# Kernel optimization log

Measured on AMD Instinct MI355X. Metric: run time of the kernel, lower is better.

Reference implementation:

```python
import jax, jax.numpy as jnp
import numpy as np

B, T, C, H = 2, 2048, 1024, 16
D = C // H  # head dim 64

def setup_inputs() -> dict:
    key = jax.random.key(0)
    k1, k2, k3 = jax.random.split(key, 3)
    x = jax.random.normal(k1, (B, T, C), dtype=jnp.float32)
    W_attn = jax.random.normal(k2, (C, 3 * C), dtype=jnp.float32) * (1.0 / np.sqrt(C))
    b_attn = jnp.zeros((3 * C,), dtype=jnp.float32)
    W_proj = jax.random.normal(k3, (C, C), dtype=jnp.float32) * (1.0 / np.sqrt(C))
    b_proj = jnp.zeros((C,), dtype=jnp.float32)
    return {"x": x, "W_attn": W_attn, "b_attn": b_attn, "W_proj": W_proj, "b_proj": b_proj}

def reference(x, W_attn, b_attn, W_proj, b_proj):
    Bsz, Tlen, Cdim = x.shape
    qkv = x @ W_attn + b_attn  # [B,T,3C]
    q, k, v = jnp.split(qkv, 3, axis=2)
    # [B,T,C] -> [B,H,T,D]
    q = q.reshape(Bsz, Tlen, H, D).transpose(0, 2, 1, 3)
    k = k.reshape(Bsz, Tlen, H, D).transpose(0, 2, 1, 3)
    v = v.reshape(Bsz, Tlen, H, D).transpose(0, 2, 1, 3)
    att = jnp.einsum('bhqd,bhkd->bhqk', q, k) * (1.0 / np.sqrt(D))
    causal = jnp.tril(jnp.ones((Tlen, Tlen), dtype=bool))
    att = jnp.where(causal[None, None, :, :], att, jnp.float32(-jnp.inf))
    att = jax.nn.softmax(att, axis=-1)
    y = jnp.einsum('bhqk,bhkd->bhqd', att, v)  # [B,H,T,D]
    y = y.transpose(0, 2, 1, 3).reshape(Bsz, Tlen, Cdim)
    return y @ W_proj + b_proj
```

## Files before the change

kernel.cpp:

```cpp
#include <hip/hip_runtime.h>
#include <math.h>

#define BSZ 2
#define TSEQ 2048
#define CDIM 1024
#define HNUM 16

typedef __attribute__((ext_vector_type(8))) short bhalf8;
typedef __attribute__((ext_vector_type(4))) short bhalf4;
typedef __attribute__((ext_vector_type(4))) float floatx4;

__device__ __forceinline__ unsigned short f2bf(float f) {
    union { float f; unsigned u; } v;
    v.f = f;
    unsigned r = v.u + 0x7FFFu + ((v.u >> 16) & 1u);
    return (unsigned short)(r >> 16);
}

__device__ __forceinline__ floatx4 fx4_zero() { floatx4 z = {0.f,0.f,0.f,0.f}; return z; }

typedef __attribute__((address_space(3))) unsigned int lds_u32;
typedef const __attribute__((address_space(1))) unsigned int g_u32;
__device__ __forceinline__ void async_copy16(const void* g, void* l) {
    __builtin_amdgcn_global_load_lds((g_u32*)g, (lds_u32*)l, 16, 0, 0);
}

__device__ __forceinline__ void trans_tile(
    const float* __restrict__ W, unsigned short* __restrict__ Wt,
    int K, int N, int n0, int k0, int tid, float (*t)[33])
{
    const int tx = tid & 31, ty = tid >> 5;
#pragma unroll
    for (int i = 0; i < 4; ++i)
        t[ty + i * 8][tx] = W[(size_t)(k0 + ty + i * 8) * N + n0 + tx];
    __syncthreads();
#pragma unroll
    for (int i = 0; i < 4; ++i)
        Wt[(size_t)(n0 + ty + i * 8) * K + k0 + tx] = f2bf(t[tx][ty + i * 8]);
}

__global__ __launch_bounds__(256) void prepass(
    const float* __restrict__ x, unsigned short* __restrict__ xb,
    const float* __restrict__ Wa, unsigned short* __restrict__ WtA,
    const float* __restrict__ Wp, unsigned short* __restrict__ WtP)
{
    __shared__ float t[32][33];
    const int bid = blockIdx.x;
    const int tid = threadIdx.x;
    if (bid < 2048) {
        size_t i = ((size_t)bid * 256 + tid) * 8;
        float4 a = *(const float4*)(x + i);
        float4 b = *(const float4*)(x + i + 4);
        uint4 o;
        o.x = (unsigned)f2bf(a.x) | ((unsigned)f2bf(a.y) << 16);
        o.y = (unsigned)f2bf(a.z) | ((unsigned)f2bf(a.w) << 16);
        o.z = (unsigned)f2bf(b.x) | ((unsigned)f2bf(b.y) << 16);
        o.w = (unsigned)f2bf(b.z) | ((unsigned)f2bf(b.w) << 16);
        *(uint4*)(xb + i) = o;
    } else if (bid < 5120) {
        int tl = bid - 2048;
        trans_tile(Wa, WtA, 1024, 3072, (tl % 96) * 32, (tl / 96) * 32, tid, t);
    } else {
        int tl = bid - 5120;
        trans_tile(Wp, WtP, 1024, 1024, (tl % 32) * 32, (tl / 32) * 32, tid, t);
    }
}

template<int BM, bool OUT_BF16>
__global__ __launch_bounds__(256) void gemm_bt(
    const unsigned short* __restrict__ A, const unsigned short* __restrict__ Bt,
    const float* __restrict__ bias, void* __restrict__ Cp,
    int M, int N, int K, int v_start, unsigned short* __restrict__ vt)
{
    constexpr int ALINES = BM / 64;
    constexpr int MT = BM / 32;
    __shared__ unsigned short As[2][BM * 32];
    __shared__ unsigned short Bs[2][128 * 32];

    const int tid   = threadIdx.x;
    const int bm    = blockIdx.y;
    const int bn    = blockIdx.x;
    const int wave  = tid >> 6;
    const int col16 = tid & 15;
    const int quad  = (tid & 63) >> 4;
    const int wm    = (wave >> 1) * (BM / 2);
    const int wn    = (wave & 1) * 64;

    floatx4 acc[MT][4];
#pragma unroll
    for (int i = 0; i < MT; ++i)
#pragma unroll
        for (int j = 0; j < 4; ++j) acc[i][j] = fx4_zero();

    const int gr = tid >> 2;
    const int gk = (tid & 3) * 8;
    const unsigned short* Ab = A  + (size_t)(bm * BM + gr) * K + gk;
    const unsigned short* Bb = Bt + (size_t)(bn * 128 + gr) * K + gk;

#define STAGE(k0, bf) { \
    char* AsB = (char*)As[bf] + wave * 1024; \
    char* BsB = (char*)Bs[bf] + wave * 1024; \
    _Pragma("unroll") \
    for (int l = 0; l < ALINES; ++l) \
        async_copy16(Ab + (size_t)l * 64 * K + (k0), AsB + l * 4096); \
    async_copy16(Bb + (k0), BsB); \
    async_copy16(Bb + (size_t)64 * K + (k0), BsB + 4096); }

#define COMPUTE(bf) { \
    bhalf8 a[MT], b[4]; \
    _Pragma("unroll") \
    for (int i = 0; i < MT; ++i) \
        a[i] = *(const bhalf8*)&As[bf][(wm + i * 16 + col16) * 32 + quad * 8]; \
    _Pragma("unroll") \
    for (int j = 0; j < 4; ++j) \
        b[j] = *(const bhalf8*)&Bs[bf][(wn + j * 16 + col16) * 32 + quad * 8]; \
    _Pragma("unroll") \
    for (int i = 0; i < MT; ++i) \
        _Pragma("unroll") \
        for (int j = 0; j < 4; ++j) \
            acc[i][j] = __builtin_amdgcn_mfma_f32_16x16x32_bf16(a[i], b[j], acc[i][j], 0, 0, 0); }

    STAGE(0, 0);
    __syncthreads();
    int buf = 0;
    for (int k0 = 0; k0 < K - 32; k0 += 32) {
        STAGE(k0 + 32, buf ^ 1);
        COMPUTE(buf);
        __syncthreads();
        buf ^= 1;
    }
    COMPUTE(buf);
#undef STAGE
#undef COMPUTE

    const int colbase = bn * 128 + wn;
    const bool vpath = (v_start >= 0) && (colbase >= v_start);
#pragma unroll
    for (int j = 0; j < 4; ++j) {
        int col = colbase + j * 16 + col16;
        float bv = bias[col];
#pragma unroll
        for (int i = 0; i < MT; ++i) {
            if (vpath) {
                int row0 = bm * BM + wm + i * 16 + quad * 4;
                ushort4 o;
                o.x = f2bf(acc[i][j][0] + bv);
                o.y = f2bf(acc[i][j][1] + bv);
                o.z = f2bf(acc[i][j][2] + bv);
                o.w = f2bf(acc[i][j][3] + bv);
                size_t vrow = (size_t)((row0 >> 11) * 1024 + (col - v_start));
                *(ushort4*)(vt + vrow * 2048 + (row0 & 2047)) = o;
            } else {
#pragma unroll
                for (int r = 0; r < 4; ++r) {
                    int row = bm * BM + wm + i * 16 + quad * 4 + r;
                    float v = acc[i][j][r] + bv;
                    if (OUT_BF16)
                        ((unsigned short*)Cp)[(size_t)row * N + col] = f2bf(v);
                    else
                        ((float*)Cp)[(size_t)row * N + col] = v;
                }
            }
        }
    }
}

template<bool DIAG>
__device__ __forceinline__ void attn_tile(
    const unsigned short* __restrict__ Ks, const unsigned short* __restrict__ Vt,
    const bhalf8* qf, floatx4* oT, float& l_part,
    int col16, int quad, int qloc)
{
    const float C_MUL = 0.125f * 1.44269504f;
    const float C_SUB = 17.31234049f;
    const int sx = col16 & 7;

    floatx4 s[4];
#pragma unroll
    for (int n = 0; n < 4; ++n) {
        const int row = 16 * n + col16;
        bhalf8 k0 = *(const bhalf8*)&Ks[row * 64 + ((quad ^ sx) * 8)];
        bhalf8 k1 = *(const bhalf8*)&Ks[row * 64 + (((4 + quad) ^ sx) * 8)];
        floatx4 t = __builtin_amdgcn_mfma_f32_16x16x32_bf16(k0, qf[0], fx4_zero(), 0, 0, 0);
        s[n] = __builtin_amdgcn_mfma_f32_16x16x32_bf16(k1, qf[1], t, 0, 0, 0);
    }

    bhalf4 pb[4];
#pragma unroll
    for (int n = 0; n < 4; ++n) {
        unsigned a[4];
#pragma unroll
        for (int r = 0; r < 4; ++r) {
            float p = exp2f(fmaf(s[n][r], C_MUL, -C_SUB));
            if (DIAG) {
                if (16 * n + quad * 4 + r > qloc) p = 0.f;
            }
            l_part += p;
            a[r] = __float_as_uint(p) + 0x8000u;
        }
        union { unsigned u[2]; bhalf4 b; } uu;
        uu.u[0] = (a[0] >> 16) | (a[1] & 0xffff0000u);
        uu.u[1] = (a[2] >> 16) | (a[3] & 0xffff0000u);
        pb[n] = uu.b;
    }

#pragma unroll
    for (int n = 0; n < 4; ++n) {
#pragma unroll
        for (int dt = 0; dt < 4; ++dt) {
            const int d = 16 * dt + col16;
            const bhalf4 av = *(const bhalf4*)&Vt[d * 76 + 16 * n + quad * 4];
            oT[dt] = __builtin_amdgcn_mfma_f32_16x16x16bf16_1k(av, pb[n], oT[dt], 0, 0, 0);
        }
    }
}

__global__ __launch_bounds__(256) void attn_mfma(
    const unsigned short* __restrict__ qkv,
    const unsigned short* __restrict__ vT,
    unsigned short* __restrict__ yout)
{
    __shared__ unsigned short Kbuf[2][64 * 64];
    __shared__ unsigned short Vbuf[2][64 * 76];

    const int tid   = threadIdx.x;
    const int wave  = tid >> 6;
    const int col16 = tid & 15;
    const int quad  = (tid & 63) >> 4;
    const int qb    = (int)gridDim.y - 1 - (int)blockIdx.y;
    const int bh    = blockIdx.x;
    const int b     = bh >> 4;
    const int h     = bh & 15;

    const unsigned short* base  = qkv + (size_t)b * TSEQ * 3072 + h * 64;
    const unsigned short* kbase = base + CDIM;
    const unsigned short* vtb   = vT + (size_t)(b * 1024 + h * 64) * 2048;

    bhalf8 qf[2];
    {
        const unsigned short* qrow =
            base + (size_t)(qb * 64 + wave * 16 + col16) * 3072 + quad * 8;
        qf[0] = *(const bhalf8*)qrow;
        qf[1] = *(const bhalf8*)(qrow + 32);
    }

    const int krow = tid >> 3;
    const int kchk = (tid & 7) ^ (krow & 7);
    const unsigned short* ksrc0 = kbase + (size_t)krow * 3072 + kchk * 8;
    const unsigned short* ksrc1 = kbase + (size_t)(krow + 32) * 3072 + kchk * 8;

    const int vd  = tid >> 3;
    const int vt0 = (tid & 7) * 8;
    const unsigned short* vsrc0 = vtb + (size_t)vd * 2048 + vt0;
    const unsigned short* vsrc1 = vtb + (size_t)(vd + 32) * 2048 + vt0;

#define KSTAGE(kb, bf) { \
    char* Kd = (char*)Kbuf[bf] + wave * 1024; \
    async_copy16(ksrc0 + (size_t)(kb) * 64 * 3072, Kd); \
    async_copy16(ksrc1 + (size_t)(kb) * 64 * 3072, Kd + 4096); }

    floatx4 oT[4];
#pragma unroll
    for (int dt = 0; dt < 4; ++dt) oT[dt] = fx4_zero();
    float l_part = 0.f;
    const int qloc = wave * 16 + col16;

    {
        uint4 nv0 = *(const uint4*)vsrc0;
        uint4 nv1 = *(const uint4*)vsrc1;
        KSTAGE(0, 0);
        *(uint4*)&Vbuf[0][vd * 76 + vt0]        = nv0;
        *(uint4*)&Vbuf[0][(vd + 32) * 76 + vt0] = nv1;
    }
    __syncthreads();
    int buf = 0;
    for (int kb = 0; kb < qb; ++kb) {
        uint4 nv0 = *(const uint4*)(vsrc0 + (size_t)(kb + 1) * 64);
        uint4 nv1 = *(const uint4*)(vsrc1 + (size_t)(kb + 1) * 64);
        KSTAGE(kb + 1, buf ^ 1);
        attn_tile<false>(Kbuf[buf], Vbuf[buf], qf, oT, l_part, col16, quad, qloc);
        *(uint4*)&Vbuf[buf ^ 1][vd * 76 + vt0]        = nv0;
        *(uint4*)&Vbuf[buf ^ 1][(vd + 32) * 76 + vt0] = nv1;
        __syncthreads();
        buf ^= 1;
    }
    attn_tile<true>(Kbuf[buf], Vbuf[buf], qf, oT, l_part, col16, quad, qloc);
#undef KSTAGE

    float l = l_part;
    l += __shfl_xor(l, 16);
    l += __shfl_xor(l, 32);
    const float inv = 1.0f / l;
    const size_t row = (size_t)b * TSEQ + (size_t)qb * 64 + wave * 16 + col16;
#pragma unroll
    for (int dt = 0; dt < 4; ++dt) {
        ushort4 o;
        o.x = f2bf(oT[dt][0] * inv);
        o.y = f2bf(oT[dt][1] * inv);
        o.z = f2bf(oT[dt][2] * inv);
        o.w = f2bf(oT[dt][3] * inv);
        *(ushort4*)(yout + row * CDIM + h * 64 + 16 * dt + quad * 4) = o;
    }
}

extern "C" void kernel_launch(void* const* d_in, const int* in_sizes, int n_in,
                              void* d_out, int out_size, void* d_ws, size_t ws_size,
                              hipStream_t stream)
{
    const float* x      = (const float*)d_in[0];
    const float* W_attn = (const float*)d_in[1];
    const float* b_attn = (const float*)d_in[2];
    const float* W_proj = (const float*)d_in[3];
    const float* b_proj = (const float*)d_in[4];
    float* out = (float*)d_out;

    unsigned short* qkv = (unsigned short*)d_ws;
    unsigned short* y   = qkv + (size_t)4096 * 3072;
    unsigned short* xb  = y   + (size_t)4096 * 1024;
    unsigned short* WtA = xb  + (size_t)4096 * 1024;
    unsigned short* WtP = WtA + (size_t)3072 * 1024;
    unsigned short* vT  = WtP + (size_t)1024 * 1024;

    prepass<<<dim3(6144), 256, 0, stream>>>(x, xb, W_attn, WtA, W_proj, WtP);

    gemm_bt<128, true><<<dim3(3072 / 128, 4096 / 128), 256, 0, stream>>>(
        xb, WtA, b_attn, qkv, 4096, 3072, 1024, 2048, vT);

    attn_mfma<<<dim3(BSZ * HNUM, TSEQ / 64), 256, 0, stream>>>(qkv, vT, y);

    gemm_bt<64, false><<<dim3(1024 / 128, 4096 / 64), 256, 0, stream>>>(
        y, WtP, b_proj, out, 4096, 1024, 1024, -1, nullptr);
}
```

Measured before the change: 181.6 us.

## Compute softmax row sums via MFMA with ones and use packed FMA and perm

Replaces the per-element scalar accumulation of the softmax denominator with an extra MFMA per key block that multiplies a ones vector by the bf16 probabilities, which also removes the cross-lane shuffle reduction at the end. The exponent argument is computed with packed two-wide float math, and the bf16 packing uses a byte-permute instruction (truncation instead of round-to-nearest). This moves VALU work onto the matrix unit at the cost of four more MFMAs per tile. The row sum is now taken over bf16-rounded probabilities, which changes numerics slightly.

New measurement: 185.5 us. 2.2% more time.

```diff
diff --git a/kernel.cpp b/kernel.cpp
--- a/kernel.cpp
+++ b/kernel.cpp
@@ -9,6 +9,7 @@
 typedef __attribute__((ext_vector_type(8))) short bhalf8;
 typedef __attribute__((ext_vector_type(4))) short bhalf4;
 typedef __attribute__((ext_vector_type(4))) float floatx4;
+typedef __attribute__((ext_vector_type(2))) float floatx2;
 
 __device__ __forceinline__ unsigned short f2bf(float f) {
     union { float f; unsigned u; } v;
@@ -168,7 +169,7 @@
 template<bool DIAG>
 __device__ __forceinline__ void attn_tile(
     const unsigned short* __restrict__ Ks, const unsigned short* __restrict__ Vt,
-    const bhalf8* qf, floatx4* oT, float& l_part,
+    const bhalf8* qf, floatx4* oT, floatx4& oL,
     int col16, int quad, int qloc)
 {
     const float C_MUL = 0.125f * 1.44269504f;
@@ -188,21 +189,33 @@
     bhalf4 pb[4];
 #pragma unroll
     for (int n = 0; n < 4; ++n) {
-        unsigned a[4];
-#pragma unroll
-        for (int r = 0; r < 4; ++r) {
-            float p = exp2f(fmaf(s[n][r], C_MUL, -C_SUB));
-            if (DIAG) {
-                if (16 * n + quad * 4 + r > qloc) p = 0.f;
-            }
-            l_part += p;
-            a[r] = __float_as_uint(p) + 0x8000u;
+        floatx2 a01 = {s[n][0], s[n][1]};
+        floatx2 a23 = {s[n][2], s[n][3]};
+        a01 = a01 * C_MUL - C_SUB;
+        a23 = a23 * C_MUL - C_SUB;
+        float p0 = exp2f(a01[0]);
+        float p1 = exp2f(a01[1]);
+        float p2 = exp2f(a23[0]);
+        float p3 = exp2f(a23[1]);
+        if (DIAG) {
+            const int kv0 = 16 * n + quad * 4;
+            if (kv0 + 0 > qloc) p0 = 0.f;
+            if (kv0 + 1 > qloc) p1 = 0.f;
+            if (kv0 + 2 > qloc) p2 = 0.f;
+            if (kv0 + 3 > qloc) p3 = 0.f;
         }
+        unsigned u0 = __builtin_amdgcn_perm(__float_as_uint(p1), __float_as_uint(p0), 0x07060302u);
+        unsigned u1 = __builtin_amdgcn_perm(__float_as_uint(p3), __float_as_uint(p2), 0x07060302u);
         union { unsigned u[2]; bhalf4 b; } uu;
-        uu.u[0] = (a[0] >> 16) | (a[1] & 0xffff0000u);
-        uu.u[1] = (a[2] >> 16) | (a[3] & 0xffff0000u);
+        uu.u[0] = u0;
+        uu.u[1] = u1;
         pb[n] = uu.b;
     }
+
+    const bhalf4 ones = {(short)0x3F80, (short)0x3F80, (short)0x3F80, (short)0x3F80};
+#pragma unroll
+    for (int n = 0; n < 4; ++n)
+        oL = __builtin_amdgcn_mfma_f32_16x16x16bf16_1k(ones, pb[n], oL, 0, 0, 0);
 
 #pragma unroll
     for (int n = 0; n < 4; ++n) {
@@ -262,7 +275,7 @@
     floatx4 oT[4];
 #pragma unroll
     for (int dt = 0; dt < 4; ++dt) oT[dt] = fx4_zero();
-    float l_part = 0.f;
+    floatx4 oL = fx4_zero();
     const int qloc = wave * 16 + col16;
 
     {
@@ -278,19 +291,16 @@
         uint4 nv0 = *(const uint4*)(vsrc0 + (size_t)(kb + 1) * 64);
         uint4 nv1 = *(const uint4*)(vsrc1 + (size_t)(kb + 1) * 64);
         KSTAGE(kb + 1, buf ^ 1);
-        attn_tile<false>(Kbuf[buf], Vbuf[buf], qf, oT, l_part, col16, quad, qloc);
+        attn_tile<false>(Kbuf[buf], Vbuf[buf], qf, oT, oL, col16, quad, qloc);
         *(uint4*)&Vbuf[buf ^ 1][vd * 76 + vt0]        = nv0;
         *(uint4*)&Vbuf[buf ^ 1][(vd + 32) * 76 + vt0] = nv1;
         __syncthreads();
         buf ^= 1;
     }
-    attn_tile<true>(Kbuf[buf], Vbuf[buf], qf, oT, l_part, col16, quad, qloc);
+    attn_tile<true>(Kbuf[buf], Vbuf[buf], qf, oT, oL, col16, quad, qloc);
 #undef KSTAGE
 
-    float l = l_part;
-    l += __shfl_xor(l, 16);
-    l += __shfl_xor(l, 32);
-    const float inv = 1.0f / l;
+    const float inv = 1.0f / oL[0];
     const size_t row = (size_t)b * TSEQ + (size_t)qb * 64 + wave * 16 + col16;
 #pragma unroll
     for (int dt = 0; dt < 4; ++dt) {
```
